# Kernel tuning notes

Measured on AMD Instinct MI355X. Metric: run time of the kernel, lower is better.

Reference implementation:

```python
import jax, jax.numpy as jnp
import numpy as np

M = 8        # number of input features
NMF = 4      # membership functions per feature
R = NMF ** M # 65536 rules
N = 1024     # batch size


def setup_inputs() -> dict:
    key = jax.random.key(0)
    k1, k2, k3, k4, k5 = jax.random.split(key, 5)
    x = jax.random.normal(k1, (N, M), dtype=jnp.float32)
    # Antecedent parameters: torch.rand -> uniform [0,1)
    center = jax.random.uniform(k2, (M, NMF), dtype=jnp.float32)
    sigma = jax.random.uniform(k3, (M, NMF), dtype=jnp.float32)
    # Consequent linear layer, init_Consequent uses uniform [0,1)
    W = jax.random.uniform(k4, (R, M), dtype=jnp.float32)
    b = jax.random.uniform(k5, (R,), dtype=jnp.float32)
    return {"x": x, "center": center, "sigma": sigma, "W": W, "b": b}


def reference(x, center, sigma, W, b):
    # droprule=False (deterministic reference; the torch drop_rule is random Bernoulli masking)
    n = x.shape[0]
    # Gaussian membership, faithful to torch: exp(-(x - c)^2 / 2 * sigma^2)
    # mg: [N, M, NMF]
    mg = jnp.exp(-((x[:, :, None] - center[None, :, :]) ** 2) * 0.5 * (sigma[None, :, :] ** 2))
    # Combinatorial rule product via mixed-radix broadcasting:
    # fg[n, r] = prod_m mg[n, m, digit_m(r)], feature 0 most significant.
    fg = mg[:, 0, :]  # [N, NMF]
    for m in range(1, M):
        fg = (fg[:, :, None] * mg[:, m, None, :]).reshape(n, -1)
    # fg: [N, R]
    fg_bar = fg / jnp.sum(fg, axis=1, keepdims=True)
    rule_out = x @ W.T + b  # [N, R]
    return jnp.sum(fg_bar * rule_out, axis=1)  # [N]
```

## Files before the change

kernel.cpp:

```cpp
#include <hip/hip_runtime.h>

typedef __attribute__((ext_vector_type(8))) short short8;
typedef __attribute__((ext_vector_type(4))) float f32x4;

#define KB 16
#define ROWP 16

__global__ __launch_bounds__(256) void fz_main(
    const float* __restrict__ x, const float* __restrict__ center,
    const float* __restrict__ sigma, const float* __restrict__ W,
    const float* __restrict__ b, float* __restrict__ S , int N)
{
    __shared__ float  mgs[16][33];
    __shared__ float  pr[16][20];
    __shared__ ushort plf[8][64][8];
    __shared__ float  phs[16][17];
    __shared__ float  red[4][16][9];

    const int t = threadIdx.x;
    const int tile = blockIdx.x >> 4;
    const int kb = blockIdx.x & (KB - 1);

    #pragma unroll
    for (int v = 0; v < 2; ++v) {
        int id = t + v * 256;
        int s = id >> 5, i = id & 31, m = i >> 2;
        float xv = x[(size_t)(tile * 16 + s) * 8 + m];
        float d = xv - center[i];
        float sg = sigma[i];
        mgs[s][i] = __expf(-d * d * 0.5f * sg * sg);
    }
    __syncthreads();
    {
        int s = t >> 4, a = t & 15;
        pr[s][a] = mgs[s][24 + (a >> 2)] * mgs[s][28 + (a & 3)];
        int hi = kb * KB + a;
        phs[s][a] = mgs[s][hi >> 6] * mgs[s][4 + ((hi >> 4) & 3)]
                  * mgs[s][8 + ((hi >> 2) & 3)] * mgs[s][12 + (hi & 3)];
    }
    __syncthreads();
    {
        const int ls = t >> 5;
        #pragma unroll
        for (int oct = 0; oct < 2; ++oct) {
            const int lane_e = (2 * t + oct) & 63;
            const int s = lane_e & 15;
            const int hi3 = lane_e >> 4;
            const int L0 = ls * 32 + hi3 * 8;
            const float pqv = mgs[s][16 + (L0 >> 6)] * mgs[s][20 + ((L0 >> 4) & 3)];
            const int b7 = L0 & 8;
            const float4 r0 = *reinterpret_cast<const float4*>(&pr[s][b7]);
            const float4 r1 = *reinterpret_cast<const float4*>(&pr[s][b7 + 4]);
            float pv[8] = { pqv * r0.x, pqv * r0.y, pqv * r0.z, pqv * r0.w,
                            pqv * r1.x, pqv * r1.y, pqv * r1.z, pqv * r1.w };
            unsigned Pk[4];
            #pragma unroll
            for (int j2 = 0; j2 < 4; ++j2) {
                union { float f; unsigned u; } a0, a1;
                a0.f = pv[2 * j2]; a1.f = pv[2 * j2 + 1];
                Pk[j2] = ((a0.u + 0x8000u) >> 16) | ((a1.u + 0x8000u) & 0xFFFF0000u);
            }
            *reinterpret_cast<short8*>(&plf[ls][lane_e][0]) =
                *reinterpret_cast<short8*>(&Pk[0]);
        }
    }
    __syncthreads();

    const int wv = t >> 6, lane = t & 63;
    const int c = lane & 15, kb4 = lane >> 4;
    short8 A[8];
    #pragma unroll
    for (int ls = 0; ls < 8; ++ls)
        A[ls] = *reinterpret_cast<const short8*>(&plf[ls][lane][0]);

    const float* src = (c < 8) ? (W + c) : b;
    const int stride = (c < 8) ? 8 : 1;
    const unsigned lmask = (c <= 8) ? 0xFFFFFFFFu : 0u;

    const int hi_base = kb * KB + wv * 4;
    const float* p = src + (size_t)(hi_base * 256 + kb4 * 8) * stride;
    const ptrdiff_t s32 = (ptrdiff_t)32 * stride;

    float buf[2][8];
    #pragma unroll
    for (int j = 0; j < 8; ++j) buf[0][j] = p[j * stride];

    f32x4 master = {0.f, 0.f, 0.f, 0.f};
    f32x4 d = {0.f, 0.f, 0.f, 0.f};
    #pragma unroll
    for (int step = 0; step < 32; ++step) {
        const float* pn = p + s32;
        if (step < 31) {
            #pragma unroll
            for (int j = 0; j < 8; ++j) buf[(step + 1) & 1][j] = pn[j * stride];
        }
        const float* cu = buf[step & 1];
        unsigned Bp[4];
        #pragma unroll
        for (int j2 = 0; j2 < 4; ++j2) {
            union { float f; unsigned u; } a0, a1;
            a0.f = cu[2 * j2]; a1.f = cu[2 * j2 + 1];
            Bp[j2] = (((a0.u + 0x8000u) >> 16) | ((a1.u + 0x8000u) & 0xFFFF0000u)) & lmask;
        }
        short8 B = *reinterpret_cast<short8*>(&Bp[0]);
        d = __builtin_amdgcn_mfma_f32_16x16x32_bf16(A[step & 7], B, d, 0, 0, 0);
        if ((step & 7) == 7) {
            const int hil = step >> 3;
            #pragma unroll
            for (int r = 0; r < 4; ++r)
                master[r] += phs[kb4 * 4 + r][wv * 4 + hil] * d[r];
            d = (f32x4){0.f, 0.f, 0.f, 0.f};
        }
        p = pn;
    }

    if (c < 9) {
        #pragma unroll
        for (int r = 0; r < 4; ++r)
            red[wv][kb4 * 4 + r][c] = master[r];
    }
    __syncthreads();
    if (t < 144) {
        int s = t / 9, cc = t % 9;
        float v = red[0][s][cc] + red[1][s][cc] + red[2][s][cc] + red[3][s][cc];
        S[((size_t)kb * N + tile * 16 + s) * ROWP + cc] = v;
    }
}

__global__ __launch_bounds__(64) void fz_final(
    const float* __restrict__ x, const float* __restrict__ center,
    const float* __restrict__ sigma, const float* __restrict__ S,
    float* __restrict__ out, int N)
{
    int n = blockIdx.x * 64 + threadIdx.x;
    if (n >= N) return;
    float xv[8];
    #pragma unroll
    for (int m = 0; m < 8; ++m) xv[m] = x[(size_t)n * 8 + m];
    float denom = 1.f;
    #pragma unroll
    for (int m = 0; m < 8; ++m) {
        float ssum = 0.f;
        #pragma unroll
        for (int j = 0; j < 4; ++j) {
            float dd = xv[m] - center[m * 4 + j];
            float sg = sigma[m * 4 + j];
            ssum += __expf(-dd * dd * 0.5f * sg * sg);
        }
        denom *= ssum;
    }
    float sc[9];
    #pragma unroll
    for (int cc = 0; cc < 9; ++cc) sc[cc] = 0.f;
    #pragma unroll
    for (int ch = 0; ch < KB; ++ch) {
        const float* p = S + ((size_t)ch * N + n) * ROWP;
        const float4 a  = *reinterpret_cast<const float4*>(p);
        const float4 bq = *reinterpret_cast<const float4*>(p + 4);
        sc[0] += a.x;  sc[1] += a.y;  sc[2] += a.z;  sc[3] += a.w;
        sc[4] += bq.x; sc[5] += bq.y; sc[6] += bq.z; sc[7] += bq.w;
        sc[8] += p[8];
    }
    float num = sc[8];
    #pragma unroll
    for (int m = 0; m < 8; ++m) num += xv[m] * sc[m];
    out[n] = num / denom;
}

extern "C" void kernel_launch(void* const* d_in, const int* in_sizes, int n_in,
                              void* d_out, int out_size, void* d_ws, size_t ws_size,
                              hipStream_t stream)
{
    const float* x      = (const float*)d_in[0];
    const float* center = (const float*)d_in[1];
    const float* sigma  = (const float*)d_in[2];
    const float* W      = (const float*)d_in[3];
    const float* b      = (const float*)d_in[4];
    float* out = (float*)d_out;
    const int N = in_sizes[0] / 8;

    float* S = (float*)d_ws;

    fz_main<<<(N / 16) * KB, 256, 0, stream>>>(x, center, sigma, W, b, S, N);
    fz_final<<<(N + 63) / 64, 64, 0, stream>>>(x, center, sigma, S, out, N);
}
```

Before: 76.67 us.

## Split rule dimension across twice as many blocks and load A fragments from LDS per step

Doubles the number of rule chunks per sample tile (KB 16→32) so each block covers half as many high-order rule groups, halving the per-wave MFMA loop length and doubling grid size. A fragments are now read from shared memory each step instead of held in eight registers, and launch bounds request higher occupancy. The bf16 conversion uses the library intrinsic instead of manual rounding. The cost is more blocks redundantly computing membership tables and more partial sums for the final kernel to reduce.

```diff
diff --git a/kernel.cpp b/kernel.cpp
--- a/kernel.cpp
+++ b/kernel.cpp
@@ -1,24 +1,34 @@
 #include <hip/hip_runtime.h>
+#include <hip/hip_bf16.h>
 
 typedef __attribute__((ext_vector_type(8))) short short8;
 typedef __attribute__((ext_vector_type(4))) float f32x4;
 
-#define KB 16
+#define KB 32
+#define HPB 8
 #define ROWP 16
 
-__global__ __launch_bounds__(256) void fz_main(
+__device__ __forceinline__ ushort f2bf(float f) {
+    __hip_bfloat16 h = __float2bfloat16(f);
+    return *reinterpret_cast<ushort*>(&h);
+}
+__device__ __forceinline__ unsigned pk2(float a, float b) {
+    return (unsigned)f2bf(a) | ((unsigned)f2bf(b) << 16);
+}
+
+__global__ __launch_bounds__(256, 8) void fz_main(
     const float* __restrict__ x, const float* __restrict__ center,
     const float* __restrict__ sigma, const float* __restrict__ W,
     const float* __restrict__ b, float* __restrict__ S , int N)
 {
     __shared__ float  mgs[16][33];
-    __shared__ float  pr[16][20];
-    __shared__ ushort plf[8][64][8];
-    __shared__ float  phs[16][17];
+    __shared__ float  pr[16][20] __attribute__((aligned(16)));
+    __shared__ ushort plf[8][64][8] __attribute__((aligned(16)));
+    __shared__ float  phs[16][HPB + 1];
     __shared__ float  red[4][16][9];
 
     const int t = threadIdx.x;
-    const int tile = blockIdx.x >> 4;
+    const int tile = blockIdx.x >> 5;
     const int kb = blockIdx.x & (KB - 1);
 
     #pragma unroll
@@ -34,9 +44,11 @@
     {
         int s = t >> 4, a = t & 15;
         pr[s][a] = mgs[s][24 + (a >> 2)] * mgs[s][28 + (a & 3)];
-        int hi = kb * KB + a;
-        phs[s][a] = mgs[s][hi >> 6] * mgs[s][4 + ((hi >> 4) & 3)]
-                  * mgs[s][8 + ((hi >> 2) & 3)] * mgs[s][12 + (hi & 3)];
+        if (a < HPB) {
+            int hi = kb * HPB + a;
+            phs[s][a] = mgs[s][hi >> 6] * mgs[s][4 + ((hi >> 4) & 3)]
+                      * mgs[s][8 + ((hi >> 2) & 3)] * mgs[s][12 + (hi & 3)];
+        }
     }
     __syncthreads();
     {
@@ -51,15 +63,8 @@
             const int b7 = L0 & 8;
             const float4 r0 = *reinterpret_cast<const float4*>(&pr[s][b7]);
             const float4 r1 = *reinterpret_cast<const float4*>(&pr[s][b7 + 4]);
-            float pv[8] = { pqv * r0.x, pqv * r0.y, pqv * r0.z, pqv * r0.w,
-                            pqv * r1.x, pqv * r1.y, pqv * r1.z, pqv * r1.w };
-            unsigned Pk[4];
-            #pragma unroll
-            for (int j2 = 0; j2 < 4; ++j2) {
-                union { float f; unsigned u; } a0, a1;
-                a0.f = pv[2 * j2]; a1.f = pv[2 * j2 + 1];
-                Pk[j2] = ((a0.u + 0x8000u) >> 16) | ((a1.u + 0x8000u) & 0xFFFF0000u);
-            }
+            unsigned Pk[4] = { pk2(pqv * r0.x, pqv * r0.y), pk2(pqv * r0.z, pqv * r0.w),
+                               pk2(pqv * r1.x, pqv * r1.y), pk2(pqv * r1.z, pqv * r1.w) };
             *reinterpret_cast<short8*>(&plf[ls][lane_e][0]) =
                 *reinterpret_cast<short8*>(&Pk[0]);
         }
@@ -68,47 +73,40 @@
 
     const int wv = t >> 6, lane = t & 63;
     const int c = lane & 15, kb4 = lane >> 4;
-    short8 A[8];
-    #pragma unroll
-    for (int ls = 0; ls < 8; ++ls)
-        A[ls] = *reinterpret_cast<const short8*>(&plf[ls][lane][0]);
 
     const float* src = (c < 8) ? (W + c) : b;
     const int stride = (c < 8) ? 8 : 1;
     const unsigned lmask = (c <= 8) ? 0xFFFFFFFFu : 0u;
 
-    const int hi_base = kb * KB + wv * 4;
+    const int hi_base = kb * HPB + wv * 2;
     const float* p = src + (size_t)(hi_base * 256 + kb4 * 8) * stride;
     const ptrdiff_t s32 = (ptrdiff_t)32 * stride;
 
-    float buf[2][8];
+    float bufA[8], bufB[8];
     #pragma unroll
-    for (int j = 0; j < 8; ++j) buf[0][j] = p[j * stride];
+    for (int j = 0; j < 8; ++j) bufA[j] = p[j * stride];
 
     f32x4 master = {0.f, 0.f, 0.f, 0.f};
     f32x4 d = {0.f, 0.f, 0.f, 0.f};
     #pragma unroll
-    for (int step = 0; step < 32; ++step) {
+    for (int step = 0; step < 16; ++step) {
         const float* pn = p + s32;
-        if (step < 31) {
+        float* nxt = (step & 1) ? bufA : bufB;
+        if (step < 15) {
             #pragma unroll
-            for (int j = 0; j < 8; ++j) buf[(step + 1) & 1][j] = pn[j * stride];
+            for (int j = 0; j < 8; ++j) nxt[j] = pn[j * stride];
         }
-        const float* cu = buf[step & 1];
-        unsigned Bp[4];
-        #pragma unroll
-        for (int j2 = 0; j2 < 4; ++j2) {
-            union { float f; unsigned u; } a0, a1;
-            a0.f = cu[2 * j2]; a1.f = cu[2 * j2 + 1];
-            Bp[j2] = (((a0.u + 0x8000u) >> 16) | ((a1.u + 0x8000u) & 0xFFFF0000u)) & lmask;
-        }
+        const float* cu = (step & 1) ? bufB : bufA;
+        unsigned Bp[4] = { pk2(cu[0], cu[1]) & lmask, pk2(cu[2], cu[3]) & lmask,
+                           pk2(cu[4], cu[5]) & lmask, pk2(cu[6], cu[7]) & lmask };
         short8 B = *reinterpret_cast<short8*>(&Bp[0]);
-        d = __builtin_amdgcn_mfma_f32_16x16x32_bf16(A[step & 7], B, d, 0, 0, 0);
+        short8 A = *reinterpret_cast<const short8*>(&plf[step & 7][lane][0]);
+        d = __builtin_amdgcn_mfma_f32_16x16x32_bf16(A, B, d, 0, 0, 0);
         if ((step & 7) == 7) {
             const int hil = step >> 3;
             #pragma unroll
             for (int r = 0; r < 4; ++r)
-                master[r] += phs[kb4 * 4 + r][wv * 4 + hil] * d[r];
+                master[r] += phs[kb4 * 4 + r][wv * 2 + hil] * d[r];
             d = (f32x4){0.f, 0.f, 0.f, 0.f};
         }
         p = pn;
```

Measured after the change: 79.90 us. 4.2% more time.
